# Optimization experiments

Measured on AMD Instinct MI355X. Metric: run time of the kernel, lower is better.

Reference implementation:

```python
import jax, jax.numpy as jnp
import numpy as np

BS, NE, F = 128, 512, 6
HEADS, DPH = 4, 4
N_EMBD = HEADS * DPH  # 16


def setup_inputs() -> dict:
    key = jax.random.key(0)
    k_inp, k_mask, kq, kk, kv, kp = jax.random.split(key, 6)
    inp = jax.random.normal(k_inp, (BS, NE, F), dtype=jnp.float32)
    # binary float mask; guarantee at least one unmasked entity per batch row
    mask = (jax.random.uniform(k_mask, (BS, NE)) < 0.8).astype(jnp.float32)
    mask = mask.at[:, 0].set(1.0)
    std = 1.0 / np.sqrt(N_EMBD)
    Wq = jax.random.normal(kq, (N_EMBD, F), dtype=jnp.float32) * std
    Wk = jax.random.normal(kk, (N_EMBD, F), dtype=jnp.float32) * std
    Wv = jax.random.normal(kv, (N_EMBD, F), dtype=jnp.float32) * std
    Wpost = jax.random.normal(kp, (F, N_EMBD), dtype=jnp.float32) * std
    return {"inp": inp, "mask": mask, "Wq": Wq, "Wk": Wk, "Wv": Wv, "Wpost": Wpost}


def reference(inp, mask, Wq, Wk, Wv, Wpost):
    bs, ne, f = inp.shape
    x_in = inp * mask[:, :, None]                       # mask input entities
    # projections (Linear with weight [out,in]): x @ W.T
    q = (x_in @ Wq.T).reshape(bs, ne, HEADS, DPH)
    k = (x_in @ Wk.T).reshape(bs, ne, HEADS, DPH)
    v = (x_in @ Wv.T).reshape(bs, ne, HEADS, DPH)
    scale = 1.0 / np.sqrt(N_EMBD / HEADS)               # 1/sqrt(4)
    logits = jnp.einsum('bqhd,bkhd->bhqk', q, k) * scale  # [bs,H,NE,NE]
    logits = logits + 1e9 * (mask[:, None, None, :] - 1.0)  # mask keys pre-softmax
    p = jax.nn.softmax(logits, axis=-1)
    p = p * mask[:, None, :, None]                      # zero masked query rows
    att = jnp.einsum('bhqk,bkhd->bqhd', p, v).reshape(bs, ne, N_EMBD)
    x = x_in + att @ Wpost.T                            # residual
    # mask-corrected mean/std normalization over dims [1,2]
    N = jnp.sum(mask, axis=1)[:, None, None]            # [bs,1,1] valid entity count
    mu = jnp.mean(x, axis=(1, 2), keepdims=True) * (ne / N)
    x2 = x + (1.0 - mask[:, :, None]) * mu              # fill masked slots with mu
    m2 = jnp.mean(x2, axis=(1, 2), keepdims=True)
    var = jnp.sum((x2 - m2) ** 2, axis=(1, 2), keepdims=True) / (ne * f - 1)  # unbiased
    std = jnp.sqrt(var) * jnp.sqrt((f * ne - 1.0) / (f * N - 1.0))
    xn = (x - mu) / (std + 1e-6)
    # masked mean pool over entities
    summed = jnp.sum(xn * mask[:, :, None], axis=1)     # [bs,F]
    denom = jnp.sum(mask, axis=1)[:, None]
    return summed / denom
```

## Files before the change

kernel.cpp:

```cpp
#include <hip/hip_runtime.h>
#include <math.h>

#define BS    128
#define NE    512
#define F     6
#define NH    4
#define DPH   4
#define NEMBD 16

#define CH    8
#define CPAD  65

#if __has_builtin(__builtin_amdgcn_exp2f)
#define EXP2(x) __builtin_amdgcn_exp2f(x)
#else
#define EXP2(x) exp2f(x)
#endif

typedef float v2f __attribute__((ext_vector_type(2)));

__global__ __launch_bounds__(512) void attn_kernel(
    const float* __restrict__ inp, const float* __restrict__ mask,
    const float* __restrict__ Wq, const float* __restrict__ Wk,
    const float* __restrict__ Wv, float* __restrict__ att_out)
{
    const int b    = blockIdx.x >> 2;
    const int h    = blockIdx.x & 3;
    const int t    = threadIdx.x;
    const int c    = t & 7;
    const int g    = t >> 3;
    const int w    = t >> 6;
    const int lane = t & 63;

    __shared__ float4 sk[CH * CPAD];
    __shared__ float4 sv[CH * CPAD];
    __shared__ float4 sq[576];
    __shared__ unsigned short rlist[512];
    __shared__ int scnt;
    __shared__ int swb[8];

    const float4 z4 = make_float4(0.f, 0.f, 0.f, 0.f);
    sk[c * CPAD + g] = z4;
    sv[c * CPAD + g] = z4;
    sq[9 * g + c]    = z4;
    if (t == 0) scnt = 0;

    const float me = mask[b * NE + t];
    const bool act = me > 0.f;

    __syncthreads();

    const unsigned long long ball = __ballot(act);
    const unsigned int blo = (unsigned int)ball;
    const unsigned int bhi = (unsigned int)(ball >> 32);
    const int prefix = __builtin_amdgcn_mbcnt_hi(bhi,
                        __builtin_amdgcn_mbcnt_lo(blo, 0));
    if (lane == 0) swb[w] = atomicAdd(&scnt, (int)__popcll(ball));

    __syncthreads();

    const int Nk = scnt;
    const int L  = (Nk + 7) >> 3;
    const float lcorr = (float)(8 * L - Nk);

    if (act) {
        const int s = swb[w] + prefix;
        const float2* rp = (const float2*)(inp + ((size_t)(b * NE + t)) * F);
        const float2 r0 = rp[0], r1 = rp[1], r2 = rp[2];
        const float x0 = r0.x, x1 = r0.y, x2 = r1.x,
                    x3 = r1.y, x4 = r2.x, x5 = r2.y;
        const float* wk = Wk + h * DPH * F;
        const float* wv = Wv + h * DPH * F;
        const float* wq = Wq + h * DPH * F;
        const float QS = 0.5f * 1.44269504088896340736f;
        float kk[4], vv[4], qq[4];
        #pragma unroll
        for (int d = 0; d < DPH; ++d) {
            const float* wd = wk + d * F;
            kk[d] = x0*wd[0] + x1*wd[1] + x2*wd[2] + x3*wd[3] + x4*wd[4] + x5*wd[5];
            wd = wv + d * F;
            vv[d] = x0*wd[0] + x1*wd[1] + x2*wd[2] + x3*wd[3] + x4*wd[4] + x5*wd[5];
            wd = wq + d * F;
            qq[d] = QS * (x0*wd[0] + x1*wd[1] + x2*wd[2] + x3*wd[3] + x4*wd[4] + x5*wd[5]);
        }
        sk[(s & 7) * CPAD + (s >> 3)] = make_float4(kk[0], kk[1], kk[2], kk[3]);
        sv[(s & 7) * CPAD + (s >> 3)] = make_float4(vv[0], vv[1], vv[2], vv[3]);
        sq[9 * (s >> 3) + (s & 7)]    = make_float4(qq[0], qq[1], qq[2], qq[3]);
        rlist[s] = (unsigned short)t;
    }

    __syncthreads();

    if (64 * w >= Nk) return;

    float4 qa[8];
    #pragma unroll
    for (int r = 0; r < 8; ++r) qa[r] = sq[9 * g + r];
    v2f qv[4][DPH];
    #pragma unroll
    for (int p = 0; p < 4; ++p) {
        qv[p][0] = (v2f){qa[2*p].x, qa[2*p+1].x};
        qv[p][1] = (v2f){qa[2*p].y, qa[2*p+1].y};
        qv[p][2] = (v2f){qa[2*p].z, qa[2*p+1].z};
        qv[p][3] = (v2f){qa[2*p].w, qa[2*p+1].w};
    }

    const float4* kb = sk + c * CPAD;
    const float4* vb = sv + c * CPAD;
    v2f l2[4], a2[4][DPH];
    #pragma unroll
    for (int p = 0; p < 4; ++p) {
        l2[p] = (v2f)(0.f);
        #pragma unroll
        for (int d = 0; d < DPH; ++d) a2[p][d] = (v2f)(0.f);
    }

    #pragma unroll 4
    for (int j = 0; j < L; ++j) {
        const float4 kv = kb[j];
        const float4 uv = vb[j];
        const v2f kx = (v2f){kv.x, kv.x}, ky = (v2f){kv.y, kv.y},
                  kz = (v2f){kv.z, kv.z}, kw = (v2f){kv.w, kv.w};
        const v2f ux = (v2f){uv.x, uv.x}, uy = (v2f){uv.y, uv.y},
                  uz = (v2f){uv.z, uv.z}, uw = (v2f){uv.w, uv.w};
        #pragma unroll
        for (int p = 0; p < 4; ++p) {
            v2f s = qv[p][3] * kw;
            s = __builtin_elementwise_fma(qv[p][2], kz, s);
            s = __builtin_elementwise_fma(qv[p][1], ky, s);
            s = __builtin_elementwise_fma(qv[p][0], kx, s);
            v2f e;
            e.x = EXP2(s.x);
            e.y = EXP2(s.y);
            l2[p] += e;
            a2[p][0] = __builtin_elementwise_fma(e, ux, a2[p][0]);
            a2[p][1] = __builtin_elementwise_fma(e, uy, a2[p][1]);
            a2[p][2] = __builtin_elementwise_fma(e, uz, a2[p][2]);
            a2[p][3] = __builtin_elementwise_fma(e, uw, a2[p][3]);
        }
    }

    #pragma unroll
    for (int m = 1; m <= 4; m <<= 1) {
        #pragma unroll
        for (int p = 0; p < 4; ++p) {
            l2[p].x += __shfl_xor(l2[p].x, m);
            l2[p].y += __shfl_xor(l2[p].y, m);
            #pragma unroll
            for (int d = 0; d < DPH; ++d) {
                a2[p][d].x += __shfl_xor(a2[p][d].x, m);
                a2[p][d].y += __shfl_xor(a2[p][d].y, m);
            }
        }
    }

    float lsel = l2[0].x, p0 = a2[0][0].x, p1 = a2[0][1].x,
          p2 = a2[0][2].x, p3 = a2[0][3].x;
    #pragma unroll
    for (int r = 1; r < 8; ++r) {
        if (r == c) {
            const int pp = r >> 1;
            if (r & 1) {
                lsel = l2[pp].y; p0 = a2[pp][0].y; p1 = a2[pp][1].y;
                p2 = a2[pp][2].y; p3 = a2[pp][3].y;
            } else {
                lsel = l2[pp].x; p0 = a2[pp][0].x; p1 = a2[pp][1].x;
                p2 = a2[pp][2].x; p3 = a2[pp][3].x;
            }
        }
    }

    const int slot = 8 * g + c;
    if (slot < Nk) {
        const int row = rlist[slot];
        const float rs = 1.0f / (lsel - lcorr);
        float4* o = (float4*)(att_out + ((size_t)(b * NE + row)) * NEMBD + h * DPH);
        *o = make_float4(p0 * rs, p1 * rs, p2 * rs, p3 * rs);
    }
}

__global__ __launch_bounds__(NE) void epi_kernel(
    const float* __restrict__ inp, const float* __restrict__ mask,
    const float* __restrict__ Wpost, const float* __restrict__ att,
    float* __restrict__ out)
{
    const int b = blockIdx.x;
    const int i = threadIdx.x;
    const int wave = i >> 6;
    const int lane = i & 63;

    __shared__ float swp[F * NEMBD];
    __shared__ float red[64];

    if (i < F * NEMBD) swp[i] = Wpost[i];
    __syncthreads();

    const float mi = mask[b * NE + i];
    const float* row = inp + ((size_t)(b * NE + i)) * F;
    const float* ar  = att + ((size_t)(b * NE + i)) * NEMBD;

    float a[NEMBD];
    #pragma unroll
    for (int t = 0; t < NEMBD; t += 4) {
        const float4 v = *(const float4*)(ar + t);
        a[t] = v.x * mi; a[t+1] = v.y * mi; a[t+2] = v.z * mi; a[t+3] = v.w * mi;
    }

    float x[F];
    #pragma unroll
    for (int f = 0; f < F; ++f) {
        float acc = row[f] * mi;
        #pragma unroll
        for (int t = 0; t < NEMBD; ++t) acc = fmaf(a[t], swp[f * NEMBD + t], acc);
        x[f] = acc;
    }

    float rsum = x[0] + x[1] + x[2] + x[3] + x[4] + x[5];
    float rn = mi;
    #pragma unroll
    for (int off = 32; off >= 1; off >>= 1) {
        rsum += __shfl_down(rsum, off);
        rn   += __shfl_down(rn, off);
    }
    if (lane == 0) { red[wave * 2] = rsum; red[wave * 2 + 1] = rn; }
    __syncthreads();
    float S = 0.f, N = 0.f;
    #pragma unroll
    for (int w = 0; w < 8; ++w) { S += red[w * 2]; N += red[w * 2 + 1]; }

    const float mu     = S / (6.0f * N);
    const float sum_x2 = S + (NE - N) * 6.0f * mu;
    const float m2     = sum_x2 / (NE * 6.0f);
    const float add    = (1.0f - mi) * mu;

    float ss = 0.f;
    #pragma unroll
    for (int f = 0; f < F; ++f) { const float d = x[f] + add - m2; ss = fmaf(d, d, ss); }

    __syncthreads();
    #pragma unroll
    for (int off = 32; off >= 1; off >>= 1) ss += __shfl_down(ss, off);
    if (lane == 0) red[wave] = ss;
    __syncthreads();
    float vs = 0.f;
    #pragma unroll
    for (int w = 0; w < 8; ++w) vs += red[w];

    const float var  = vs / (NE * 6.0f - 1.0f);
    const float stdv = sqrtf(var) * sqrtf((6.0f * NE - 1.0f) / (6.0f * N - 1.0f));
    const float inv  = 1.0f / (stdv + 1e-6f);

    float y[F];
    #pragma unroll
    for (int f = 0; f < F; ++f) y[f] = mi * (x[f] - mu) * inv;

    __syncthreads();
    #pragma unroll
    for (int off = 32; off >= 1; off >>= 1) {
        #pragma unroll
        for (int f = 0; f < F; ++f) y[f] += __shfl_down(y[f], off);
    }
    if (lane == 0) {
        #pragma unroll
        for (int f = 0; f < F; ++f) red[wave * F + f] = y[f];
    }
    __syncthreads();
    if (i < F) {
        float tt = 0.f;
        #pragma unroll
        for (int w = 0; w < 8; ++w) tt += red[w * F + i];
        out[b * F + i] = tt / N;
    }
}

extern "C" void kernel_launch(void* const* d_in, const int* in_sizes, int n_in,
                              void* d_out, int out_size, void* d_ws, size_t ws_size,
                              hipStream_t stream) {
    const float* inp   = (const float*)d_in[0];
    const float* mask  = (const float*)d_in[1];
    const float* Wq    = (const float*)d_in[2];
    const float* Wk    = (const float*)d_in[3];
    const float* Wv    = (const float*)d_in[4];
    const float* Wpost = (const float*)d_in[5];
    float* out = (float*)d_out;
    float* att = (float*)d_ws;

    attn_kernel<<<BS * NH, 512, 0, stream>>>(inp, mask, Wq, Wk, Wv, att);
    epi_kernel <<<BS, NE, 0, stream>>>(inp, mask, Wpost, att, out);
}
```

Baseline: 95.45 us.

## Split attention keys across two blocks per head and merge partials in epilogue

Each (batch, head) attention block is split into two blocks, each handling half of the key waves, which doubles the grid. Each block computes K/V only for its own half of the keys and writes unnormalized partial outputs plus partial softmax denominators to the workspace. The epilogue sums the two partials and normalizes them. The aim is more parallelism and shorter per-block key loops on the GPU. In exchange, workspace traffic roughly doubles, and the merge is correct only if both halves use the same exponent offset.

```diff
diff --git a/kernel.cpp b/kernel.cpp
--- a/kernel.cpp
+++ b/kernel.cpp
@@ -9,7 +9,7 @@
 #define NEMBD 16
 
 #define CH    8
-#define CPAD  65
+#define CPAD  33
 
 #if __has_builtin(__builtin_amdgcn_exp2f)
 #define EXP2(x) __builtin_amdgcn_exp2f(x)
@@ -22,10 +22,12 @@
 __global__ __launch_bounds__(512) void attn_kernel(
     const float* __restrict__ inp, const float* __restrict__ mask,
     const float* __restrict__ Wq, const float* __restrict__ Wk,
-    const float* __restrict__ Wv, float* __restrict__ att_out)
+    const float* __restrict__ Wv,
+    float4* __restrict__ attp, float* __restrict__ lp)
 {
-    const int b    = blockIdx.x >> 2;
-    const int h    = blockIdx.x & 3;
+    const int b    = blockIdx.x >> 3;
+    const int h    = (blockIdx.x >> 1) & 3;
+    const int kh   = blockIdx.x & 1;
     const int t    = threadIdx.x;
     const int c    = t & 7;
     const int g    = t >> 3;
@@ -36,57 +38,68 @@
     __shared__ float4 sv[CH * CPAD];
     __shared__ float4 sq[576];
     __shared__ unsigned short rlist[512];
-    __shared__ int scnt;
-    __shared__ int swb[8];
+    __shared__ int wcnt[8];
 
     const float4 z4 = make_float4(0.f, 0.f, 0.f, 0.f);
-    sk[c * CPAD + g] = z4;
-    sv[c * CPAD + g] = z4;
-    sq[9 * g + c]    = z4;
-    if (t == 0) scnt = 0;
+    if (t < CH * CPAD) { sk[t] = z4; sv[t] = z4; }
+    sq[9 * g + c] = z4;
 
     const float me = mask[b * NE + t];
     const bool act = me > 0.f;
 
-    __syncthreads();
-
     const unsigned long long ball = __ballot(act);
-    const unsigned int blo = (unsigned int)ball;
-    const unsigned int bhi = (unsigned int)(ball >> 32);
-    const int prefix = __builtin_amdgcn_mbcnt_hi(bhi,
-                        __builtin_amdgcn_mbcnt_lo(blo, 0));
-    if (lane == 0) swb[w] = atomicAdd(&scnt, (int)__popcll(ball));
-
-    __syncthreads();
-
-    const int Nk = scnt;
-    const int L  = (Nk + 7) >> 3;
-    const float lcorr = (float)(8 * L - Nk);
+    const int prefix = __builtin_amdgcn_mbcnt_hi((unsigned int)(ball >> 32),
+                        __builtin_amdgcn_mbcnt_lo((unsigned int)ball, 0));
+    if (lane == 0) wcnt[w] = (int)__popcll(ball);
+
+    __syncthreads();
+
+    int rbase = 0, Nk = 0, Nk_h = 0, kbase = 0;
+    #pragma unroll
+    for (int u = 0; u < 8; ++u) {
+        const int cu = wcnt[u];
+        Nk += cu;
+        if (u < w) rbase += cu;
+        if ((u >> 2) == kh) {
+            Nk_h += cu;
+            if (u < w) kbase += cu;
+        }
+    }
+    const int L = (Nk_h + 7) >> 3;
+    const float padcorr = (float)(8 * L - Nk_h);
 
     if (act) {
-        const int s = swb[w] + prefix;
+        const int s = rbase + prefix;
         const float2* rp = (const float2*)(inp + ((size_t)(b * NE + t)) * F);
         const float2 r0 = rp[0], r1 = rp[1], r2 = rp[2];
         const float x0 = r0.x, x1 = r0.y, x2 = r1.x,
                     x3 = r1.y, x4 = r2.x, x5 = r2.y;
-        const float* wk = Wk + h * DPH * F;
-        const float* wv = Wv + h * DPH * F;
+        const float QS = 0.5f * 1.44269504088896340736f;
         const float* wq = Wq + h * DPH * F;
-        const float QS = 0.5f * 1.44269504088896340736f;
-        float kk[4], vv[4], qq[4];
+        float qq[4];
         #pragma unroll
         for (int d = 0; d < DPH; ++d) {
-            const float* wd = wk + d * F;
-            kk[d] = x0*wd[0] + x1*wd[1] + x2*wd[2] + x3*wd[3] + x4*wd[4] + x5*wd[5];
-            wd = wv + d * F;
-            vv[d] = x0*wd[0] + x1*wd[1] + x2*wd[2] + x3*wd[3] + x4*wd[4] + x5*wd[5];
-            wd = wq + d * F;
+            const float* wd = wq + d * F;
             qq[d] = QS * (x0*wd[0] + x1*wd[1] + x2*wd[2] + x3*wd[3] + x4*wd[4] + x5*wd[5]);
         }
-        sk[(s & 7) * CPAD + (s >> 3)] = make_float4(kk[0], kk[1], kk[2], kk[3]);
-        sv[(s & 7) * CPAD + (s >> 3)] = make_float4(vv[0], vv[1], vv[2], vv[3]);
-        sq[9 * (s >> 3) + (s & 7)]    = make_float4(qq[0], qq[1], qq[2], qq[3]);
+        sq[9 * (s >> 3) + (s & 7)] = make_float4(qq[0], qq[1], qq[2], qq[3]);
         rlist[s] = (unsigned short)t;
+
+        if ((w >> 2) == kh) {
+            const int ks = kbase + prefix;
+            const float* wk = Wk + h * DPH * F;
+            const float* wv = Wv + h * DPH * F;
+            float kk[4], vv[4];
+            #pragma unroll
+            for (int d = 0; d < DPH; ++d) {
+                const float* wd = wk + d * F;
+                kk[d] = x0*wd[0] + x1*wd[1] + x2*wd[2] + x3*wd[3] + x4*wd[4] + x5*wd[5];
+                wd = wv + d * F;
+                vv[d] = x0*wd[0] + x1*wd[1] + x2*wd[2] + x3*wd[3] + x4*wd[4] + x5*wd[5];
+            }
+            sk[(ks & 7) * CPAD + (ks >> 3)] = make_float4(kk[0], kk[1], kk[2], kk[3]);
+            sv[(ks & 7) * CPAD + (ks >> 3)] = make_float4(vv[0], vv[1], vv[2], vv[3]);
+        }
     }
 
     __syncthreads();
@@ -173,15 +186,16 @@
     const int slot = 8 * g + c;
     if (slot < Nk) {
         const int row = rlist[slot];
-        const float rs = 1.0f / (lsel - lcorr);
-        float4* o = (float4*)(att_out + ((size_t)(b * NE + row)) * NEMBD + h * DPH);
-        *o = make_float4(p0 * rs, p1 * rs, p2 * rs, p3 * rs);
+        const size_t idx = (((size_t)(b * NE + row)) * NH + h) * 2 + kh;
+        attp[idx] = make_float4(p0, p1, p2, p3);
+        lp[idx]   = lsel - padcorr;
     }
 }
 
 __global__ __launch_bounds__(NE) void epi_kernel(
     const float* __restrict__ inp, const float* __restrict__ mask,
-    const float* __restrict__ Wpost, const float* __restrict__ att,
+    const float* __restrict__ Wpost,
+    const float4* __restrict__ attp, const float* __restrict__ lpa,
     float* __restrict__ out)
 {
     const int b = blockIdx.x;
@@ -197,13 +211,19 @@
 
     const float mi = mask[b * NE + i];
     const float* row = inp + ((size_t)(b * NE + i)) * F;
-    const float* ar  = att + ((size_t)(b * NE + i)) * NEMBD;
+    const float4* ap = attp + ((size_t)(b * NE + i)) * NH * 2;
+    const float*  lr = lpa  + ((size_t)(b * NE + i)) * NH * 2;
 
     float a[NEMBD];
     #pragma unroll
-    for (int t = 0; t < NEMBD; t += 4) {
-        const float4 v = *(const float4*)(ar + t);
-        a[t] = v.x * mi; a[t+1] = v.y * mi; a[t+2] = v.z * mi; a[t+3] = v.w * mi;
+    for (int h = 0; h < NH; ++h) {
+        const float4 s0 = ap[2 * h], s1 = ap[2 * h + 1];
+        const float  l  = lr[2 * h] + lr[2 * h + 1];
+        const float  sc = mi / l;
+        a[4*h+0] = (s0.x + s1.x) * sc;
+        a[4*h+1] = (s0.y + s1.y) * sc;
+        a[4*h+2] = (s0.z + s1.z) * sc;
+        a[4*h+3] = (s0.w + s1.w) * sc;
     }
 
     float x[F];
@@ -283,8 +303,10 @@
     const float* Wv    = (const float*)d_in[4];
     const float* Wpost = (const float*)d_in[5];
     float* out = (float*)d_out;
-    float* att = (float*)d_ws;
-
-    attn_kernel<<<BS * NH, 512, 0, stream>>>(inp, mask, Wq, Wk, Wv, att);
-    epi_kernel <<<BS, NE, 0, stream>>>(inp, mask, Wpost, att, out);
+
+    float4* attp = (float4*)d_ws;
+    float*  lp   = (float*)((char*)d_ws + (size_t)BS * NE * NH * 2 * sizeof(float4));
+
+    attn_kernel<<<BS * NH * 2, 512, 0, stream>>>(inp, mask, Wq, Wk, Wv, attp, lp);
+    epi_kernel <<<BS, NE, 0, stream>>>(inp, mask, Wpost, attp, lp, out);
 }
```

Result: slower. 101.3 us (+6.1%).

## Split QKV projection into separate kernel and halve attention blocks by query rows

Applied to the files above, without the earlier changes.

Moves the Q/K/V projection and active-entity compaction into a new per-batch kernel that writes compacted Q, K, V, a row list and a count to workspace. The attention kernel now runs 256-thread blocks, two per batch and head, each handling half the query rows, and loads the shared K and V from global memory. This aims for more parallel blocks and less redundant per-head projection work. In exchange it adds a kernel launch and a global-memory round trip for Q, K and V.

```diff
diff --git a/kernel.cpp b/kernel.cpp
--- a/kernel.cpp
+++ b/kernel.cpp
@@ -19,83 +19,120 @@
 
 typedef float v2f __attribute__((ext_vector_type(2)));
 
-__global__ __launch_bounds__(512) void attn_kernel(
+__global__ __launch_bounds__(NE) void qkv_kernel(
     const float* __restrict__ inp, const float* __restrict__ mask,
     const float* __restrict__ Wq, const float* __restrict__ Wk,
-    const float* __restrict__ Wv, float* __restrict__ att_out)
+    const float* __restrict__ Wv,
+    float4* __restrict__ qc, float4* __restrict__ kc, float4* __restrict__ vc,
+    unsigned short* __restrict__ rlist, int* __restrict__ cnt)
 {
-    const int b    = blockIdx.x >> 2;
-    const int h    = blockIdx.x & 3;
+    const int b    = blockIdx.x;
     const int t    = threadIdx.x;
-    const int c    = t & 7;
-    const int g    = t >> 3;
     const int w    = t >> 6;
     const int lane = t & 63;
 
-    __shared__ float4 sk[CH * CPAD];
-    __shared__ float4 sv[CH * CPAD];
-    __shared__ float4 sq[576];
-    __shared__ unsigned short rlist[512];
-    __shared__ int scnt;
-    __shared__ int swb[8];
-
-    const float4 z4 = make_float4(0.f, 0.f, 0.f, 0.f);
-    sk[c * CPAD + g] = z4;
-    sv[c * CPAD + g] = z4;
-    sq[9 * g + c]    = z4;
-    if (t == 0) scnt = 0;
+    __shared__ int wcnt[8];
 
     const float me = mask[b * NE + t];
     const bool act = me > 0.f;
 
-    __syncthreads();
-
     const unsigned long long ball = __ballot(act);
-    const unsigned int blo = (unsigned int)ball;
-    const unsigned int bhi = (unsigned int)(ball >> 32);
-    const int prefix = __builtin_amdgcn_mbcnt_hi(bhi,
-                        __builtin_amdgcn_mbcnt_lo(blo, 0));
-    if (lane == 0) swb[w] = atomicAdd(&scnt, (int)__popcll(ball));
-
-    __syncthreads();
-
-    const int Nk = scnt;
-    const int L  = (Nk + 7) >> 3;
-    const float lcorr = (float)(8 * L - Nk);
+    const int prefix = __builtin_amdgcn_mbcnt_hi((unsigned int)(ball >> 32),
+                        __builtin_amdgcn_mbcnt_lo((unsigned int)ball, 0));
+    if (lane == 0) wcnt[w] = (int)__popcll(ball);
+    __syncthreads();
+
+    int base = 0, Nk = 0;
+    #pragma unroll
+    for (int u = 0; u < 8; ++u) {
+        const int cu = wcnt[u];
+        Nk += cu;
+        if (u < w) base += cu;
+    }
+    const int L8 = ((Nk + 7) >> 3) << 3;
 
     if (act) {
-        const int s = swb[w] + prefix;
+        const int s = base + prefix;
         const float2* rp = (const float2*)(inp + ((size_t)(b * NE + t)) * F);
         const float2 r0 = rp[0], r1 = rp[1], r2 = rp[2];
         const float x0 = r0.x, x1 = r0.y, x2 = r1.x,
                     x3 = r1.y, x4 = r2.x, x5 = r2.y;
-        const float* wk = Wk + h * DPH * F;
-        const float* wv = Wv + h * DPH * F;
-        const float* wq = Wq + h * DPH * F;
         const float QS = 0.5f * 1.44269504088896340736f;
-        float kk[4], vv[4], qq[4];
-        #pragma unroll
-        for (int d = 0; d < DPH; ++d) {
-            const float* wd = wk + d * F;
-            kk[d] = x0*wd[0] + x1*wd[1] + x2*wd[2] + x3*wd[3] + x4*wd[4] + x5*wd[5];
-            wd = wv + d * F;
-            vv[d] = x0*wd[0] + x1*wd[1] + x2*wd[2] + x3*wd[3] + x4*wd[4] + x5*wd[5];
-            wd = wq + d * F;
-            qq[d] = QS * (x0*wd[0] + x1*wd[1] + x2*wd[2] + x3*wd[3] + x4*wd[4] + x5*wd[5]);
-        }
-        sk[(s & 7) * CPAD + (s >> 3)] = make_float4(kk[0], kk[1], kk[2], kk[3]);
-        sv[(s & 7) * CPAD + (s >> 3)] = make_float4(vv[0], vv[1], vv[2], vv[3]);
-        sq[9 * (s >> 3) + (s & 7)]    = make_float4(qq[0], qq[1], qq[2], qq[3]);
-        rlist[s] = (unsigned short)t;
-    }
-
-    __syncthreads();
-
-    if (64 * w >= Nk) return;
-
+        #pragma unroll
+        for (int h = 0; h < NH; ++h) {
+            float qq[4], kk[4], vv[4];
+            #pragma unroll
+            for (int d = 0; d < DPH; ++d) {
+                const float* wd = Wq + (h * DPH + d) * F;
+                qq[d] = QS * (x0*wd[0] + x1*wd[1] + x2*wd[2] + x3*wd[3] + x4*wd[4] + x5*wd[5]);
+                wd = Wk + (h * DPH + d) * F;
+                kk[d] = x0*wd[0] + x1*wd[1] + x2*wd[2] + x3*wd[3] + x4*wd[4] + x5*wd[5];
+                wd = Wv + (h * DPH + d) * F;
+                vv[d] = x0*wd[0] + x1*wd[1] + x2*wd[2] + x3*wd[3] + x4*wd[4] + x5*wd[5];
+            }
+            const size_t o = (size_t)(b * NH + h) * NE + s;
+            qc[o] = make_float4(qq[0], qq[1], qq[2], qq[3]);
+            kc[o] = make_float4(kk[0], kk[1], kk[2], kk[3]);
+            vc[o] = make_float4(vv[0], vv[1], vv[2], vv[3]);
+        }
+        rlist[b * NE + s] = (unsigned short)t;
+    }
+
+    if (t >= Nk && t < L8) {
+        const float4 z4 = make_float4(0.f, 0.f, 0.f, 0.f);
+        #pragma unroll
+        for (int h = 0; h < NH; ++h) {
+            const size_t o = (size_t)(b * NH + h) * NE + t;
+            qc[o] = z4; kc[o] = z4; vc[o] = z4;
+        }
+    }
+    if (t == 0) cnt[b] = Nk;
+}
+
+__global__ __launch_bounds__(256) void attn_kernel(
+    const float4* __restrict__ qc, const float4* __restrict__ kc,
+    const float4* __restrict__ vc, const unsigned short* __restrict__ rlist,
+    const int* __restrict__ cnt, float* __restrict__ att)
+{
+    const int blk = blockIdx.x;
+    const int b   = blk >> 3;
+    const int h   = (blk >> 1) & 3;
+    const int rh  = blk & 1;
+    const int t   = threadIdx.x;
+    const int c   = t & 7;
+    const int g   = t >> 3;
+
+    const int Nk = cnt[b];
+    if (rh * 256 >= Nk) return;
+    const int L  = (Nk + 7) >> 3;
+    const int L8 = L << 3;
+    const float lcorr = (float)(L8 - Nk);
+
+    __shared__ float4 sk[CH * CPAD];
+    __shared__ float4 sv[CH * CPAD];
+
+    const float4* kcb = kc + (size_t)(b * NH + h) * NE;
+    const float4* vcb = vc + (size_t)(b * NH + h) * NE;
+    #pragma unroll
+    for (int s0 = 0; s0 < 2; ++s0) {
+        const int s = t + s0 * 256;
+        if (s < L8) {
+            sk[(s & 7) * CPAD + (s >> 3)] = kcb[s];
+            sv[(s & 7) * CPAD + (s >> 3)] = vcb[s];
+        }
+    }
+
+    const float4* qcb = qc + (size_t)(b * NH + h) * NE;
+    const float4 z4 = make_float4(0.f, 0.f, 0.f, 0.f);
     float4 qa[8];
     #pragma unroll
-    for (int r = 0; r < 8; ++r) qa[r] = sq[9 * g + r];
+    for (int r = 0; r < 8; ++r) {
+        const int slot = rh * 256 + 8 * g + r;
+        qa[r] = (slot < Nk) ? qcb[slot] : z4;
+    }
+
+    __syncthreads();
+
     v2f qv[4][DPH];
     #pragma unroll
     for (int p = 0; p < 4; ++p) {
@@ -170,11 +207,11 @@
         }
     }
 
-    const int slot = 8 * g + c;
+    const int slot = rh * 256 + 8 * g + c;
     if (slot < Nk) {
-        const int row = rlist[slot];
+        const int row = rlist[b * NE + slot];
         const float rs = 1.0f / (lsel - lcorr);
-        float4* o = (float4*)(att_out + ((size_t)(b * NE + row)) * NEMBD + h * DPH);
+        float4* o = (float4*)(att + ((size_t)(b * NE + row)) * NEMBD + h * DPH);
         *o = make_float4(p0 * rs, p1 * rs, p2 * rs, p3 * rs);
     }
 }
@@ -283,8 +320,17 @@
     const float* Wv    = (const float*)d_in[4];
     const float* Wpost = (const float*)d_in[5];
     float* out = (float*)d_out;
-    float* att = (float*)d_ws;
-
-    attn_kernel<<<BS * NH, 512, 0, stream>>>(inp, mask, Wq, Wk, Wv, att);
+
+    char* ws = (char*)d_ws;
+    const size_t SZQKV = (size_t)BS * NH * NE * sizeof(float4);
+    float4* qc = (float4*)(ws);
+    float4* kc = (float4*)(ws + SZQKV);
+    float4* vc = (float4*)(ws + 2 * SZQKV);
+    float*  att = (float*)(ws + 3 * SZQKV);
+    unsigned short* rlist = (unsigned short*)(ws + 4 * SZQKV);
+    int* cnt = (int*)(ws + 4 * SZQKV + (size_t)BS * NE * sizeof(unsigned short));
+
+    qkv_kernel <<<BS, NE, 0, stream>>>(inp, mask, Wq, Wk, Wv, qc, kc, vc, rlist, cnt);
+    attn_kernel<<<BS * NH * 2, 256, 0, stream>>>(qc, kc, vc, rlist, cnt, att);
     epi_kernel <<<BS, NE, 0, stream>>>(inp, mask, Wpost, att, out);
 }
```

Result: slower. 109.3 us (+14.5%).
